# Performance work log

Hardware: AMD Instinct MI355X
Metric: run time of the kernel (lower is better)

## Reference

```python
import jax, jax.numpy as jnp
import numpy as np

B, N, D = 16, 8192, 384   # examples, sentences per example, embedding dim
KN = 16                   # neighbors per node (kNN degree)
K, H, STEPS = 8, 128, 3   # coin dim, hidden dim, walk steps


def setup_inputs() -> dict:
    key = jax.random.key(0)
    ks = jax.random.split(key, 12)
    s = 0.02
    return {
        "sent_embs": jax.random.normal(ks[0], (B, N, D), dtype=jnp.float32),
        "q_embs": jax.random.normal(ks[1], (B, D), dtype=jnp.float32),
        "neighbors": jax.random.randint(ks[2], (B, N, KN), 0, N, dtype=jnp.int32),
        # coin_net: Linear(2D->H), ReLU, Linear(H->K)
        "coin_w1": jax.random.normal(ks[3], (2 * D, H), dtype=jnp.float32) * s,
        "coin_b1": jnp.zeros((H,), dtype=jnp.float32),
        "coin_w2": jax.random.normal(ks[4], (H, K), dtype=jnp.float32) * s,
        "coin_b2": jnp.zeros((K,), dtype=jnp.float32),
        # path_net: Linear(D+K+D->H), ReLU, Linear(H->1)
        "path_w1": jax.random.normal(ks[5], (D + K + D, H), dtype=jnp.float32) * s,
        "path_b1": jnp.zeros((H,), dtype=jnp.float32),
        "path_w2": jax.random.normal(ks[6], (H, 1), dtype=jnp.float32) * s,
        "path_b2": jnp.zeros((1,), dtype=jnp.float32),
    }


def _mlp(x, w1, b1, w2, b2):
    return jax.nn.relu(x @ w1 + b1) @ w2 + b2


def _forward(sent_embs, q_embs, neighbors,
             coin_w1, coin_b1, coin_w2, coin_b2,
             path_w1, path_b1, path_w2, path_b2):
    b, n, d = sent_embs.shape
    k = coin_w2.shape[1]
    q_bcast = jnp.broadcast_to(q_embs[:, None, :], (b, n, d))

    # coin amplitudes per node: [B, N, K]
    amps = _mlp(jnp.concatenate([sent_embs, q_bcast], axis=-1),
                coin_w1, coin_b1, coin_w2, coin_b2)

    # initial uniform walk state: 1/sqrt(N*K)
    state = jnp.full((b, n, k), 1.0 / np.sqrt(n * k), dtype=sent_embs.dtype)

    # adjacency = self-loop + edges row -> neighbors[row]; A @ X == X + masked neighbor gather-sum
    valid = (neighbors >= 0) & (neighbors < n)           # [B, N, KN]
    safe_nbrs = jnp.where(valid, neighbors, 0)
    batch_idx = jnp.arange(b)[:, None, None]

    for _ in range(STEPS):
        ns = state * amps                                # coin step
        gathered = ns[batch_idx, safe_nbrs]              # [B, N, KN, K]
        gathered = jnp.where(valid[..., None], gathered, 0.0)
        ns = ns + gathered.sum(axis=2)                   # sparse.mm(A, ns)
        norm = jnp.linalg.norm(ns.reshape(b, -1), axis=1)[:, None, None]
        state = ns / jnp.where(norm > 0, norm, 1.0)      # renormalize (guard norm==0)

    path_in = jnp.concatenate([sent_embs, state, q_bcast], axis=-1)  # [B, N, D+K+D]
    logits = _mlp(path_in, path_w1, path_b1, path_w2, path_b2)[..., 0]  # [B, N]
    return logits


def reference(sent_embs, q_embs, neighbors,
              coin_w1, coin_b1, coin_w2, coin_b2,
              path_w1, path_b1, path_w2, path_b2):
    return _forward(sent_embs, q_embs, neighbors,
                    coin_w1, coin_b1, coin_w2, coin_b2,
                    path_w1, path_b1, path_w2, path_b2)
```

## Files before the change

kernel.cpp:

```cpp
#include <hip/hip_runtime.h>

#define B_SZ 16
#define N_SZ 8192
#define D_SZ 384
#define KN_SZ 16
#define K_SZ 8
#define H_SZ 128
#define M_TOTAL (B_SZ * N_SZ)
#define KSTEPS 12
#define LDSA_STRIDE 392
#define MT64 (M_TOTAL / 64)
#define GEMM_GRID 512

typedef short short8 __attribute__((ext_vector_type(8)));
typedef short short4v __attribute__((ext_vector_type(4)));
typedef float floatx4 __attribute__((ext_vector_type(4)));

__device__ __forceinline__ unsigned short f2bf(float f) {
    unsigned u = __builtin_bit_cast(unsigned, f);
    u += 0x7FFFu + ((u >> 16) & 1u);
    return (unsigned short)(u >> 16);
}
__device__ __forceinline__ float bf2f(unsigned short b) {
    unsigned u = ((unsigned)b) << 16;
    return __builtin_bit_cast(float, u);
}

__global__ void prep_kernel(const float* __restrict__ q_embs,
                            const float* __restrict__ coin_w1,
                            const float* __restrict__ coin_b1,
                            const float* __restrict__ path_w1,
                            const float* __restrict__ path_b1,
                            unsigned short* __restrict__ wswz,
                            float* __restrict__ qcoin, float* __restrict__ qpath,
                            float* __restrict__ norms) {
    int blk = blockIdx.x;
    int t = threadIdx.x;
    if (blk < 384) {
        int f = blk * 256 + t;
        int j  = f & 7;
        int l  = (f >> 3) & 63;
        int ss = (f >> 9) % KSTEPS;
        int ct = f / (KSTEPS * 512);
        int k = ss * 32 + ((l >> 4) << 3) + j;
        int n = ct * 16 + (l & 15);
        float v = (n < H_SZ) ? coin_w1[k * H_SZ + n]
                             : path_w1[k * H_SZ + (n - H_SZ)];
        wswz[f] = f2bf(v);
    } else if (blk == 384) {
        if (t < B_SZ) norms[t] = 0.f;
    } else {
        int b = blk - 385;
        const float* q = q_embs + b * D_SZ;
        if (t < H_SZ) {
            float acc = coin_b1[t];
            for (int d = 0; d < D_SZ; d++)
                acc += q[d] * coin_w1[(D_SZ + d) * H_SZ + t];
            qcoin[b * H_SZ + t] = acc;
        } else if (t < 2 * H_SZ) {
            int h = t - H_SZ;
            float acc = path_b1[h];
            for (int d = 0; d < D_SZ; d++)
                acc += q[d] * path_w1[(D_SZ + K_SZ + d) * H_SZ + h];
            qpath[b * H_SZ + h] = acc;
        }
    }
}

__global__ __launch_bounds__(256, 2)
void gemm_fused(const float* __restrict__ sent,
                const unsigned short* __restrict__ wswz,
                unsigned short* __restrict__ hcoinB,
                unsigned short* __restrict__ hpathB) {
    __shared__ short als[64 * LDSA_STRIDE];
    const int tid = threadIdx.x;
    const int wave = tid >> 6, lane = tid & 63;
    const int m_lane = lane & 15, quad = lane >> 4;

    short8 bfrag[4][KSTEPS];
#pragma unroll
    for (int c = 0; c < 4; c++) {
        int ct = wave * 4 + c;
#pragma unroll
        for (int s = 0; s < KSTEPS; s++)
            bfrag[c][s] = *(const short8*)(wswz + ((((ct * KSTEPS + s) * 64) + lane) << 3));
    }

    unsigned short* dstbase = (wave < 2) ? hcoinB : hpathB;
    const int colw = (wave & 1) * 64;

    for (int mt = blockIdx.x; mt < MT64; mt += GEMM_GRID) {
        const float* abase = sent + (size_t)mt * 64 * D_SZ;
#pragma unroll
        for (int cc = 0; cc < 6; cc++) {
            float4 v[4];
#pragma unroll
            for (int u = 0; u < 4; u++)
                v[u] = *(const float4*)(abase + (size_t)((cc * 4 + u) * 256 + tid) * 4);
#pragma unroll
            for (int u = 0; u < 4; u++) {
                int e4 = (cc * 4 + u) * 256 + tid;
                int row = e4 / 96;
                int c4  = e4 - row * 96;
                short4v sv;
                sv.x = (short)f2bf(v[u].x); sv.y = (short)f2bf(v[u].y);
                sv.z = (short)f2bf(v[u].z); sv.w = (short)f2bf(v[u].w);
                *(short4v*)&als[row * LDSA_STRIDE + c4 * 4] = sv;
            }
        }
        __syncthreads();

        for (int rt = 0; rt < 4; rt++) {
            floatx4 acc[4];
#pragma unroll
            for (int c = 0; c < 4; c++) acc[c] = (floatx4){0.f, 0.f, 0.f, 0.f};
#pragma unroll
            for (int s = 0; s < KSTEPS; s++) {
                short8 afrag = *(const short8*)&als[(rt * 16 + m_lane) * LDSA_STRIDE + s * 32 + quad * 8];
#pragma unroll
                for (int c = 0; c < 4; c++)
                    acc[c] = __builtin_amdgcn_mfma_f32_16x16x32_bf16(afrag, bfrag[c][s], acc[c], 0, 0, 0);
            }
            int mt16 = mt * 4 + rt;
#pragma unroll
            for (int c = 0; c < 4; c++) {
                int col = colw + c * 16 + m_lane;
                short4v sv;
                sv.x = (short)f2bf(acc[c][0]); sv.y = (short)f2bf(acc[c][1]);
                sv.z = (short)f2bf(acc[c][2]); sv.w = (short)f2bf(acc[c][3]);
                *(short4v*)(dstbase + (size_t)mt16 * 2048 + col * 16 + quad * 4) = sv;
            }
        }
        __syncthreads();
    }
}

__global__ __launch_bounds__(256)
void amps_init_kernel(const unsigned short* __restrict__ hcoinB,
                      const float* __restrict__ qcoin,
                      const float* __restrict__ coin_w2,
                      const float* __restrict__ coin_b2,
                      float* __restrict__ amps, float* __restrict__ z0) {
    __shared__ float w2s[H_SZ * K_SZ];
    __shared__ float qcs[H_SZ];
    const int tid = threadIdx.x;
    const int m = blockIdx.x * 256 + tid;
    const int b = (blockIdx.x * 256) >> 13;
    for (int i = tid; i < H_SZ * K_SZ; i += 256) w2s[i] = coin_w2[i];
    if (tid < H_SZ) qcs[tid] = qcoin[b * H_SZ + tid];
    __syncthreads();

    const unsigned short* hb = hcoinB + (size_t)(m >> 4) * 2048 + (m & 15);
    float acc[K_SZ];
#pragma unroll
    for (int j = 0; j < K_SZ; j++) acc[j] = coin_b2[j];

    for (int h = 0; h < H_SZ; h++) {
        float hv = bf2f(hb[h * 16]) + qcs[h];
        hv = hv > 0.f ? hv : 0.f;
        float4 wa = *(const float4*)&w2s[h * 8];
        float4 wb = *(const float4*)&w2s[h * 8 + 4];
        acc[0] += hv * wa.x; acc[1] += hv * wa.y; acc[2] += hv * wa.z; acc[3] += hv * wa.w;
        acc[4] += hv * wb.x; acc[5] += hv * wb.y; acc[6] += hv * wb.z; acc[7] += hv * wb.w;
    }
    const float c0 = 1.0f / 256.0f;
    float4 o0 = {acc[0], acc[1], acc[2], acc[3]};
    float4 o1 = {acc[4], acc[5], acc[6], acc[7]};
    *(float4*)(amps + (size_t)m * 8)     = o0;
    *(float4*)(amps + (size_t)m * 8 + 4) = o1;
    float4 s0 = {acc[0]*c0, acc[1]*c0, acc[2]*c0, acc[3]*c0};
    float4 s1 = {acc[4]*c0, acc[5]*c0, acc[6]*c0, acc[7]*c0};
    *(float4*)(z0 + (size_t)m * 8)     = s0;
    *(float4*)(z0 + (size_t)m * 8 + 4) = s1;
}

__global__ __launch_bounds__(256)
void walk_step(const float* __restrict__ z,
               const int* __restrict__ neighbors,
               const float* __restrict__ amps,
               float* __restrict__ outz,
               float* __restrict__ norms, int last) {
    const int g = blockIdx.x * 256 + threadIdx.x;
    const int m = g >> 1, half = g & 1;
    const int b = m >> 13;
    const size_t nbase = (size_t)b << 13;
    const int off = half * 4;

    float4 v = *(const float4*)(z + (size_t)m * 8 + off);
    int nbr[KN_SZ];
    const int4* nb4 = (const int4*)(neighbors + (size_t)m * KN_SZ);
#pragma unroll
    for (int i = 0; i < 4; i++) *(int4*)&nbr[i * 4] = nb4[i];
#pragma unroll
    for (int i = 0; i < KN_SZ; i++) {
        int nn = nbr[i];
        if (nn >= 0 && nn < N_SZ) {
            float4 gv = *(const float4*)(z + (nbase + nn) * 8 + off);
            v.x += gv.x; v.y += gv.y; v.z += gv.z; v.w += gv.w;
        }
    }
    if (!last) {
        float4 a = *(const float4*)(amps + (size_t)m * 8 + off);
        v.x *= a.x; v.y *= a.y; v.z *= a.z; v.w *= a.w;
        *(float4*)(outz + (size_t)m * 8 + off) = v;
    } else {
        *(float4*)(outz + (size_t)m * 8 + off) = v;
        float ss = v.x * v.x + v.y * v.y + v.z * v.z + v.w * v.w;
#pragma unroll
        for (int o = 32; o > 0; o >>= 1) ss += __shfl_down(ss, o);
        __shared__ float blocksum;
        if (threadIdx.x == 0) blocksum = 0.f;
        __syncthreads();
        if ((threadIdx.x & 63) == 0) atomicAdd(&blocksum, ss);
        __syncthreads();
        if (threadIdx.x == 0) atomicAdd(&norms[b], blocksum);
    }
}

__global__ __launch_bounds__(256)
void logits_kernel(const unsigned short* __restrict__ hpathB,
                   const float* __restrict__ qpath,
                   const float* __restrict__ u2,
                   const float* __restrict__ norms,
                   const float* __restrict__ path_w1,
                   const float* __restrict__ path_w2,
                   const float* __restrict__ path_b2,
                   float* __restrict__ out) {
    __shared__ float w1t[H_SZ * K_SZ];
    __shared__ float w2s[H_SZ];
    __shared__ float qps[H_SZ];
    const int tid = threadIdx.x;
    const int m = blockIdx.x * 256 + tid;
    const int b = (blockIdx.x * 256) >> 13;
    for (int i = tid; i < H_SZ * K_SZ; i += 256) {
        int h = i >> 3, j = i & 7;
        w1t[i] = path_w1[(D_SZ + j) * H_SZ + h];
    }
    if (tid < H_SZ) { w2s[tid] = path_w2[tid]; qps[tid] = qpath[b * H_SZ + tid]; }
    __syncthreads();

    float ssq = norms[b];
    float inv = ssq > 0.f ? rsqrtf(ssq) : 1.0f;
    float st[K_SZ];
    {
        float4 s0 = *(const float4*)(u2 + (size_t)m * 8);
        float4 s1 = *(const float4*)(u2 + (size_t)m * 8 + 4);
        st[0] = s0.x * inv; st[1] = s0.y * inv; st[2] = s0.z * inv; st[3] = s0.w * inv;
        st[4] = s1.x * inv; st[5] = s1.y * inv; st[6] = s1.z * inv; st[7] = s1.w * inv;
    }

    const unsigned short* hb = hpathB + (size_t)(m >> 4) * 2048 + (m & 15);
    float acc = path_b2[0];
    for (int h = 0; h < H_SZ; h++) {
        float hv = bf2f(hb[h * 16]) + qps[h];
        float4 wa = *(const float4*)&w1t[h * 8];
        float4 wb = *(const float4*)&w1t[h * 8 + 4];
        hv += st[0]*wa.x + st[1]*wa.y + st[2]*wa.z + st[3]*wa.w
            + st[4]*wb.x + st[5]*wb.y + st[6]*wb.z + st[7]*wb.w;
        hv = hv > 0.f ? hv : 0.f;
        acc += hv * w2s[h];
    }
    out[m] = acc;
}

extern "C" void kernel_launch(void* const* d_in, const int* in_sizes, int n_in,
                              void* d_out, int out_size, void* d_ws, size_t ws_size,
                              hipStream_t stream) {
    const float* sent      = (const float*)d_in[0];
    const float* q_embs    = (const float*)d_in[1];
    const int*   neighbors = (const int*)d_in[2];
    const float* coin_w1   = (const float*)d_in[3];
    const float* coin_b1   = (const float*)d_in[4];
    const float* coin_w2   = (const float*)d_in[5];
    const float* coin_b2   = (const float*)d_in[6];
    const float* path_w1   = (const float*)d_in[7];
    const float* path_b1   = (const float*)d_in[8];
    const float* path_w2   = (const float*)d_in[9];
    const float* path_b2   = (const float*)d_in[10];
    float* out = (float*)d_out;

    char* ws = (char*)d_ws;
    unsigned short* wswz = (unsigned short*)ws;
    float* qcoin = (float*)(ws + 196608);
    float* qpath = (float*)(ws + 196608 + 8192);
    float* norms = (float*)(ws + 196608 + 16384);
    unsigned short* hcoinB = (unsigned short*)(ws + 213248);
    unsigned short* hpathB = hcoinB + (size_t)M_TOTAL * H_SZ;
    float* amps = (float*)(ws + 213248 + 2ull * 33554432ull);
    float* zA   = amps + (size_t)M_TOTAL * K_SZ;
    float* zB   = zA   + (size_t)M_TOTAL * K_SZ;

    prep_kernel<<<401, 256, 0, stream>>>(q_embs, coin_w1, coin_b1, path_w1, path_b1,
                                         wswz, qcoin, qpath, norms);
    gemm_fused<<<GEMM_GRID, 256, 0, stream>>>(sent, wswz, hcoinB, hpathB);
    amps_init_kernel<<<M_TOTAL / 256, 256, 0, stream>>>(hcoinB, qcoin, coin_w2, coin_b2, amps, zA);
    walk_step<<<2 * M_TOTAL / 256, 256, 0, stream>>>(zA, neighbors, amps, zB, norms, 0);
    walk_step<<<2 * M_TOTAL / 256, 256, 0, stream>>>(zB, neighbors, amps, zA, norms, 0);
    walk_step<<<2 * M_TOTAL / 256, 256, 0, stream>>>(zA, neighbors, amps, zB, norms, 1);
    logits_kernel<<<M_TOTAL / 256, 256, 0, stream>>>(hpathB, qpath, zB, norms,
                                                     path_w1, path_w2, path_b2, out);
}
```

Before: 421.7 us.

## Fuse coin MLP second layer into GEMM epilogue, drop hcoin buffer

The coin-branch hidden activations are now kept in an LDS tile inside the GEMM kernel, and the ReLU plus the H-to-K projection run there, writing amps and the initial walk state directly. This removes the separate amps_init kernel and the bf16 round-trip of the 32 MB hcoin buffer through global memory. The row tile shrinks from 64 to 32 rows to fit the extra shared memory, which doubles the tile count and adds two extra barriers per tile. That may reduce the block's MFMA work per synchronisation and lower occupancy.

```diff
diff --git a/kernel.cpp b/kernel.cpp
--- a/kernel.cpp
+++ b/kernel.cpp
@@ -8,8 +8,10 @@
 #define H_SZ 128
 #define M_TOTAL (B_SZ * N_SZ)
 #define KSTEPS 12
-#define LDSA_STRIDE 392
-#define MT64 (M_TOTAL / 64)
+#define TROWS 32
+#define NT (M_TOTAL / TROWS)
+#define LDSA_STRIDE 400
+#define HTS 132
 #define GEMM_GRID 512
 
 typedef short short8 __attribute__((ext_vector_type(8)));
@@ -70,13 +72,24 @@
 __global__ __launch_bounds__(256, 2)
 void gemm_fused(const float* __restrict__ sent,
                 const unsigned short* __restrict__ wswz,
-                unsigned short* __restrict__ hcoinB,
-                unsigned short* __restrict__ hpathB) {
-    __shared__ short als[64 * LDSA_STRIDE];
+                const float* __restrict__ qcoin,
+                const float* __restrict__ coin_w2,
+                const float* __restrict__ coin_b2,
+                unsigned short* __restrict__ hpathB,
+                float* __restrict__ amps,
+                float* __restrict__ z0) {
+    __shared__ short als[TROWS * LDSA_STRIDE];
+    __shared__ float htile[TROWS * HTS];
+    __shared__ float w2s[H_SZ * K_SZ];
+    __shared__ float qcs[H_SZ];
+    __shared__ float b2s[K_SZ];
     const int tid = threadIdx.x;
     const int wave = tid >> 6, lane = tid & 63;
     const int m_lane = lane & 15, quad = lane >> 4;
 
+    for (int i = tid; i < H_SZ * K_SZ; i += 256) w2s[i] = coin_w2[i];
+    if (tid < K_SZ) b2s[tid] = coin_b2[tid];
+
     short8 bfrag[4][KSTEPS];
 #pragma unroll
     for (int c = 0; c < 4; c++) {
@@ -86,13 +99,14 @@
             bfrag[c][s] = *(const short8*)(wswz + ((((ct * KSTEPS + s) * 64) + lane) << 3));
     }
 
-    unsigned short* dstbase = (wave < 2) ? hcoinB : hpathB;
     const int colw = (wave & 1) * 64;
-
-    for (int mt = blockIdx.x; mt < MT64; mt += GEMM_GRID) {
-        const float* abase = sent + (size_t)mt * 64 * D_SZ;
-#pragma unroll
-        for (int cc = 0; cc < 6; cc++) {
+    const int is_path = (wave >= 2);
+
+    for (int mt = blockIdx.x; mt < NT; mt += GEMM_GRID) {
+        const int b = mt >> 8;
+        const float* abase = sent + (size_t)mt * TROWS * D_SZ;
+#pragma unroll
+        for (int cc = 0; cc < 3; cc++) {
             float4 v[4];
 #pragma unroll
             for (int u = 0; u < 4; u++)
@@ -108,9 +122,11 @@
                 *(short4v*)&als[row * LDSA_STRIDE + c4 * 4] = sv;
             }
         }
-        __syncthreads();
-
-        for (int rt = 0; rt < 4; rt++) {
+        if (tid < H_SZ) qcs[tid] = qcoin[b * H_SZ + tid];
+        __syncthreads();
+
+#pragma unroll
+        for (int rt = 0; rt < 2; rt++) {
             floatx4 acc[4];
 #pragma unroll
             for (int c = 0; c < 4; c++) acc[c] = (floatx4){0.f, 0.f, 0.f, 0.f};
@@ -121,57 +137,65 @@
                 for (int c = 0; c < 4; c++)
                     acc[c] = __builtin_amdgcn_mfma_f32_16x16x32_bf16(afrag, bfrag[c][s], acc[c], 0, 0, 0);
             }
-            int mt16 = mt * 4 + rt;
-#pragma unroll
-            for (int c = 0; c < 4; c++) {
-                int col = colw + c * 16 + m_lane;
-                short4v sv;
-                sv.x = (short)f2bf(acc[c][0]); sv.y = (short)f2bf(acc[c][1]);
-                sv.z = (short)f2bf(acc[c][2]); sv.w = (short)f2bf(acc[c][3]);
-                *(short4v*)(dstbase + (size_t)mt16 * 2048 + col * 16 + quad * 4) = sv;
-            }
-        }
-        __syncthreads();
-    }
-}
-
-__global__ __launch_bounds__(256)
-void amps_init_kernel(const unsigned short* __restrict__ hcoinB,
-                      const float* __restrict__ qcoin,
-                      const float* __restrict__ coin_w2,
-                      const float* __restrict__ coin_b2,
-                      float* __restrict__ amps, float* __restrict__ z0) {
-    __shared__ float w2s[H_SZ * K_SZ];
-    __shared__ float qcs[H_SZ];
-    const int tid = threadIdx.x;
-    const int m = blockIdx.x * 256 + tid;
-    const int b = (blockIdx.x * 256) >> 13;
-    for (int i = tid; i < H_SZ * K_SZ; i += 256) w2s[i] = coin_w2[i];
-    if (tid < H_SZ) qcs[tid] = qcoin[b * H_SZ + tid];
-    __syncthreads();
-
-    const unsigned short* hb = hcoinB + (size_t)(m >> 4) * 2048 + (m & 15);
-    float acc[K_SZ];
-#pragma unroll
-    for (int j = 0; j < K_SZ; j++) acc[j] = coin_b2[j];
-
-    for (int h = 0; h < H_SZ; h++) {
-        float hv = bf2f(hb[h * 16]) + qcs[h];
-        hv = hv > 0.f ? hv : 0.f;
-        float4 wa = *(const float4*)&w2s[h * 8];
-        float4 wb = *(const float4*)&w2s[h * 8 + 4];
-        acc[0] += hv * wa.x; acc[1] += hv * wa.y; acc[2] += hv * wa.z; acc[3] += hv * wa.w;
-        acc[4] += hv * wb.x; acc[5] += hv * wb.y; acc[6] += hv * wb.z; acc[7] += hv * wb.w;
-    }
-    const float c0 = 1.0f / 256.0f;
-    float4 o0 = {acc[0], acc[1], acc[2], acc[3]};
-    float4 o1 = {acc[4], acc[5], acc[6], acc[7]};
-    *(float4*)(amps + (size_t)m * 8)     = o0;
-    *(float4*)(amps + (size_t)m * 8 + 4) = o1;
-    float4 s0 = {acc[0]*c0, acc[1]*c0, acc[2]*c0, acc[3]*c0};
-    float4 s1 = {acc[4]*c0, acc[5]*c0, acc[6]*c0, acc[7]*c0};
-    *(float4*)(z0 + (size_t)m * 8)     = s0;
-    *(float4*)(z0 + (size_t)m * 8 + 4) = s1;
+            if (!is_path) {
+#pragma unroll
+                for (int c = 0; c < 4; c++) {
+                    int col = colw + c * 16 + m_lane;
+#pragma unroll
+                    for (int r = 0; r < 4; r++)
+                        htile[(rt * 16 + quad * 4 + r) * HTS + col] = acc[c][r];
+                }
+            } else {
+                int mt16 = mt * 2 + rt;
+#pragma unroll
+                for (int c = 0; c < 4; c++) {
+                    int col = colw + c * 16 + m_lane;
+                    short4v sv;
+                    sv.x = (short)f2bf(acc[c][0]); sv.y = (short)f2bf(acc[c][1]);
+                    sv.z = (short)f2bf(acc[c][2]); sv.w = (short)f2bf(acc[c][3]);
+                    *(short4v*)(hpathB + (size_t)mt16 * 2048 + col * 16 + quad * 4) = sv;
+                }
+            }
+        }
+        __syncthreads();
+
+        {
+            const int row = tid >> 3, hg = tid & 7;
+            float pa[K_SZ];
+#pragma unroll
+            for (int j = 0; j < K_SZ; j++) pa[j] = 0.f;
+#pragma unroll
+            for (int k = 0; k < 16; k++) {
+                int h = hg + 8 * k;
+                float hv = htile[row * HTS + h] + qcs[h];
+                hv = hv > 0.f ? hv : 0.f;
+                float4 wa = *(const float4*)&w2s[h * 8];
+                float4 wb = *(const float4*)&w2s[h * 8 + 4];
+                pa[0] += hv * wa.x; pa[1] += hv * wa.y; pa[2] += hv * wa.z; pa[3] += hv * wa.w;
+                pa[4] += hv * wb.x; pa[5] += hv * wb.y; pa[6] += hv * wb.z; pa[7] += hv * wb.w;
+            }
+#pragma unroll
+            for (int o = 1; o < 8; o <<= 1) {
+#pragma unroll
+                for (int j = 0; j < K_SZ; j++) pa[j] += __shfl_xor(pa[j], o);
+            }
+            if ((tid & 7) == 0) {
+                const float c0 = 1.0f / 256.0f;
+                int m = mt * TROWS + row;
+#pragma unroll
+                for (int j = 0; j < K_SZ; j++) pa[j] += b2s[j];
+                float4 o0 = {pa[0], pa[1], pa[2], pa[3]};
+                float4 o1 = {pa[4], pa[5], pa[6], pa[7]};
+                *(float4*)(amps + (size_t)m * 8)     = o0;
+                *(float4*)(amps + (size_t)m * 8 + 4) = o1;
+                float4 s0 = {pa[0]*c0, pa[1]*c0, pa[2]*c0, pa[3]*c0};
+                float4 s1 = {pa[4]*c0, pa[5]*c0, pa[6]*c0, pa[7]*c0};
+                *(float4*)(z0 + (size_t)m * 8)     = s0;
+                *(float4*)(z0 + (size_t)m * 8 + 4) = s1;
+            }
+        }
+        __syncthreads();
+    }
 }
 
 __global__ __launch_bounds__(256)
@@ -232,7 +256,7 @@
     const int tid = threadIdx.x;
     const int m = blockIdx.x * 256 + tid;
     const int b = (blockIdx.x * 256) >> 13;
-    for (int i = tid; i < H_SZ * K_SZ; i += 256) {
+    for (int i = tid; i < K_SZ * H_SZ; i += 256) {
         int h = i >> 3, j = i & 7;
         w1t[i] = path_w1[(D_SZ + j) * H_SZ + h];
     }
@@ -284,16 +308,15 @@
     float* qcoin = (float*)(ws + 196608);
     float* qpath = (float*)(ws + 196608 + 8192);
     float* norms = (float*)(ws + 196608 + 16384);
-    unsigned short* hcoinB = (unsigned short*)(ws + 213248);
-    unsigned short* hpathB = hcoinB + (size_t)M_TOTAL * H_SZ;
-    float* amps = (float*)(ws + 213248 + 2ull * 33554432ull);
+    unsigned short* hpathB = (unsigned short*)(ws + 213248);
+    float* amps = (float*)(ws + 213248 + 33554432ull);
     float* zA   = amps + (size_t)M_TOTAL * K_SZ;
     float* zB   = zA   + (size_t)M_TOTAL * K_SZ;
 
     prep_kernel<<<401, 256, 0, stream>>>(q_embs, coin_w1, coin_b1, path_w1, path_b1,
                                          wswz, qcoin, qpath, norms);
-    gemm_fused<<<GEMM_GRID, 256, 0, stream>>>(sent, wswz, hcoinB, hpathB);
-    amps_init_kernel<<<M_TOTAL / 256, 256, 0, stream>>>(hcoinB, qcoin, coin_w2, coin_b2, amps, zA);
+    gemm_fused<<<GEMM_GRID, 256, 0, stream>>>(sent, wswz, qcoin, coin_w2, coin_b2,
+                                              hpathB, amps, zA);
     walk_step<<<2 * M_TOTAL / 256, 256, 0, stream>>>(zA, neighbors, amps, zB, norms, 0);
     walk_step<<<2 * M_TOTAL / 256, 256, 0, stream>>>(zB, neighbors, amps, zA, norms, 0);
     walk_step<<<2 * M_TOTAL / 256, 256, 0, stream>>>(zA, neighbors, amps, zB, norms, 1);
```

New measurement: 482.7 us. 1.14x slower.

## Load GEMM A fragments directly from global memory, drop LDS staging

Applied to the files above, without the earlier changes.

The fused GEMM no longer converts a 64-row tile of sentence embeddings to bf16 in LDS behind barriers. Each wave now loads its own fp32 A fragments straight from global memory and converts them in registers. B fragments are reloaded from global memory per k-step instead of staying resident in registers. The kernel launches one block per 64-row tile instead of a persistent grid, with launch bounds raised to 4 blocks per CU. This removes LDS traffic and syncs and cuts register pressure so more blocks fit per CU, but each A element is now read by all four waves, which raises global and cache traffic.

```diff
diff --git a/kernel.cpp b/kernel.cpp
--- a/kernel.cpp
+++ b/kernel.cpp
@@ -8,12 +8,11 @@
 #define H_SZ 128
 #define M_TOTAL (B_SZ * N_SZ)
 #define KSTEPS 12
-#define LDSA_STRIDE 392
 #define MT64 (M_TOTAL / 64)
-#define GEMM_GRID 512
 
 typedef short short8 __attribute__((ext_vector_type(8)));
 typedef short short4v __attribute__((ext_vector_type(4)));
+typedef unsigned short ushort8v __attribute__((ext_vector_type(8)));
 typedef float floatx4 __attribute__((ext_vector_type(4)));
 
 __device__ __forceinline__ unsigned short f2bf(float f) {
@@ -67,71 +66,60 @@
     }
 }
 
-__global__ __launch_bounds__(256, 2)
+__global__ __launch_bounds__(256, 4)
 void gemm_fused(const float* __restrict__ sent,
                 const unsigned short* __restrict__ wswz,
                 unsigned short* __restrict__ hcoinB,
                 unsigned short* __restrict__ hpathB) {
-    __shared__ short als[64 * LDSA_STRIDE];
     const int tid = threadIdx.x;
     const int wave = tid >> 6, lane = tid & 63;
     const int m_lane = lane & 15, quad = lane >> 4;
-
-    short8 bfrag[4][KSTEPS];
-#pragma unroll
-    for (int c = 0; c < 4; c++) {
-        int ct = wave * 4 + c;
-#pragma unroll
-        for (int s = 0; s < KSTEPS; s++)
-            bfrag[c][s] = *(const short8*)(wswz + ((((ct * KSTEPS + s) * 64) + lane) << 3));
-    }
+    const int mt = blockIdx.x;
 
     unsigned short* dstbase = (wave < 2) ? hcoinB : hpathB;
     const int colw = (wave & 1) * 64;
 
-    for (int mt = blockIdx.x; mt < MT64; mt += GEMM_GRID) {
-        const float* abase = sent + (size_t)mt * 64 * D_SZ;
-#pragma unroll
-        for (int cc = 0; cc < 6; cc++) {
-            float4 v[4];
-#pragma unroll
-            for (int u = 0; u < 4; u++)
-                v[u] = *(const float4*)(abase + (size_t)((cc * 4 + u) * 256 + tid) * 4);
-#pragma unroll
-            for (int u = 0; u < 4; u++) {
-                int e4 = (cc * 4 + u) * 256 + tid;
-                int row = e4 / 96;
-                int c4  = e4 - row * 96;
-                short4v sv;
-                sv.x = (short)f2bf(v[u].x); sv.y = (short)f2bf(v[u].y);
-                sv.z = (short)f2bf(v[u].z); sv.w = (short)f2bf(v[u].w);
-                *(short4v*)&als[row * LDSA_STRIDE + c4 * 4] = sv;
-            }
-        }
-        __syncthreads();
-
+    const float* abase = sent + (size_t)mt * 64 * D_SZ + (size_t)m_lane * D_SZ + quad * 8;
+    const unsigned short* wbase = wswz + (size_t)wave * 4 * KSTEPS * 512 + lane * 8;
+
+    floatx4 acc[4][4];
+#pragma unroll
+    for (int rt = 0; rt < 4; rt++)
+#pragma unroll
+        for (int c = 0; c < 4; c++) acc[rt][c] = (floatx4){0.f, 0.f, 0.f, 0.f};
+
+    for (int s = 0; s < KSTEPS; s++) {
+        short8 bf[4];
+#pragma unroll
+        for (int c = 0; c < 4; c++)
+            bf[c] = *(const short8*)(wbase + (size_t)(c * KSTEPS + s) * 512);
+#pragma unroll
         for (int rt = 0; rt < 4; rt++) {
-            floatx4 acc[4];
-#pragma unroll
-            for (int c = 0; c < 4; c++) acc[c] = (floatx4){0.f, 0.f, 0.f, 0.f};
-#pragma unroll
-            for (int s = 0; s < KSTEPS; s++) {
-                short8 afrag = *(const short8*)&als[(rt * 16 + m_lane) * LDSA_STRIDE + s * 32 + quad * 8];
-#pragma unroll
-                for (int c = 0; c < 4; c++)
-                    acc[c] = __builtin_amdgcn_mfma_f32_16x16x32_bf16(afrag, bfrag[c][s], acc[c], 0, 0, 0);
-            }
-            int mt16 = mt * 4 + rt;
-#pragma unroll
-            for (int c = 0; c < 4; c++) {
-                int col = colw + c * 16 + m_lane;
-                short4v sv;
-                sv.x = (short)f2bf(acc[c][0]); sv.y = (short)f2bf(acc[c][1]);
-                sv.z = (short)f2bf(acc[c][2]); sv.w = (short)f2bf(acc[c][3]);
-                *(short4v*)(dstbase + (size_t)mt16 * 2048 + col * 16 + quad * 4) = sv;
-            }
-        }
-        __syncthreads();
+            const float* ap = abase + rt * 16 * D_SZ + s * 32;
+            float4 a0 = *(const float4*)ap;
+            float4 a1 = *(const float4*)(ap + 4);
+            short8 af;
+            af[0] = (short)f2bf(a0.x); af[1] = (short)f2bf(a0.y);
+            af[2] = (short)f2bf(a0.z); af[3] = (short)f2bf(a0.w);
+            af[4] = (short)f2bf(a1.x); af[5] = (short)f2bf(a1.y);
+            af[6] = (short)f2bf(a1.z); af[7] = (short)f2bf(a1.w);
+#pragma unroll
+            for (int c = 0; c < 4; c++)
+                acc[rt][c] = __builtin_amdgcn_mfma_f32_16x16x32_bf16(af, bf[c], acc[rt][c], 0, 0, 0);
+        }
+    }
+
+#pragma unroll
+    for (int rt = 0; rt < 4; rt++) {
+        int mt16 = mt * 4 + rt;
+#pragma unroll
+        for (int c = 0; c < 4; c++) {
+            int col = colw + c * 16 + m_lane;
+            short4v sv;
+            sv.x = (short)f2bf(acc[rt][c][0]); sv.y = (short)f2bf(acc[rt][c][1]);
+            sv.z = (short)f2bf(acc[rt][c][2]); sv.w = (short)f2bf(acc[rt][c][3]);
+            *(short4v*)(dstbase + (size_t)mt16 * 2048 + col * 16 + quad * 4) = sv;
+        }
     }
 }
 
@@ -232,7 +220,7 @@
     const int tid = threadIdx.x;
     const int m = blockIdx.x * 256 + tid;
     const int b = (blockIdx.x * 256) >> 13;
-    for (int i = tid; i < H_SZ * K_SZ; i += 256) {
+    for (int i = tid; i < K_SZ * H_SZ; i += 256) {
         int h = i >> 3, j = i & 7;
         w1t[i] = path_w1[(D_SZ + j) * H_SZ + h];
     }
@@ -292,7 +280,7 @@
 
     prep_kernel<<<401, 256, 0, stream>>>(q_embs, coin_w1, coin_b1, path_w1, path_b1,
                                          wswz, qcoin, qpath, norms);
-    gemm_fused<<<GEMM_GRID, 256, 0, stream>>>(sent, wswz, hcoinB, hpathB);
+    gemm_fused<<<MT64, 256, 0, stream>>>(sent, wswz, hcoinB, hpathB);
     amps_init_kernel<<<M_TOTAL / 256, 256, 0, stream>>>(hcoinB, qcoin, coin_w2, coin_b2, amps, zA);
     walk_step<<<2 * M_TOTAL / 256, 256, 0, stream>>>(zA, neighbors, amps, zB, norms, 0);
     walk_step<<<2 * M_TOTAL / 256, 256, 0, stream>>>(zB, neighbors, amps, zA, norms, 0);
```

New measurement: 458.7 us. +8.8%, slower.
